# Performance work log

Hardware: AMD Instinct MI355X
Metric: run time of the kernel (lower is better)

Reference implementation:

```python
import jax, jax.numpy as jnp
import numpy as np

B, S, P, D = 32, 128, 64, 256   # batch, seq_len, pad_size, input_size
H, NF = 128, 3                   # hidden_size, n_filters
BI = 2                           # bidirectional -> b=2
OUT = 2                          # output_size
INITRANGE = 0.05


def setup_inputs() -> dict:
    key = jax.random.key(0)
    ks = jax.random.split(key, 17)
    u = lambda k, shape: jax.random.uniform(k, shape, jnp.float32, -INITRANGE, INITRANGE)
    return {
        "inputs": jax.random.normal(ks[0], (B, S, P, D), jnp.float32),
        "inputs_demoip": jax.random.normal(ks[1], (B, 3), jnp.float32),
        # Conv1d(1,1,kernel=D) collapses to a single dot product + scalar bias
        "conv_w": u(ks[2], (D,)),
        "conv_b": u(ks[3], ()),
        # Conv1d(1,NF,kernel=H*BI) collapses to NF dot products + bias
        "conv2_w": u(ks[4], (NF, H * BI)),
        "conv2_b": u(ks[5], (NF,)),
        # GRU params, forward and backward directions (PyTorch gate order r,z,n)
        "W_ih_f": u(ks[6], (3 * H, D)),
        "W_hh_f": u(ks[7], (3 * H, H)),
        "b_ih_f": u(ks[8], (3 * H,)),
        "b_hh_f": u(ks[9], (3 * H,)),
        "W_ih_b": u(ks[10], (3 * H, D)),
        "W_hh_b": u(ks[11], (3 * H, H)),
        "b_ih_b": u(ks[12], (3 * H,)),
        "b_hh_b": u(ks[13], (3 * H,)),
        "lin_w": u(ks[14], (OUT, H * BI * NF + 3)),
        "lin_b": u(ks[15], (OUT,)),
        "batch_size": B,
    }


def _gru_dir(x_seq, W_ih, W_hh, b_ih, b_hh, reverse):
    """Single-direction GRU, PyTorch semantics. x_seq: [B,S,D] -> [B,S,H]."""
    xg = jnp.einsum('bsd,gd->bsg', x_seq, W_ih) + b_ih  # [B,S,3H] precomputed input gates

    def step(h, xg_t):
        hg = h @ W_hh.T + b_hh
        xr, xz, xn = jnp.split(xg_t, 3, axis=-1)
        hr, hz, hn = jnp.split(hg, 3, axis=-1)
        r = jax.nn.sigmoid(xr + hr)
        z = jax.nn.sigmoid(xz + hz)
        n = jnp.tanh(xn + r * hn)
        h_new = (1.0 - z) * n + z * h
        return h_new, h_new

    h0 = jnp.zeros((x_seq.shape[0], W_hh.shape[1]), x_seq.dtype)
    _, hs = jax.lax.scan(step, h0, jnp.swapaxes(xg, 0, 1), reverse=reverse)
    return jnp.swapaxes(hs, 0, 1)


def reference(inputs, inputs_demoip, conv_w, conv_b, conv2_w, conv2_b,
              W_ih_f, W_hh_f, b_ih_f, b_hh_f,
              W_ih_b, W_hh_b, b_ih_b, b_hh_b,
              lin_w, lin_b, batch_size):
    # --- convolutional attention pooling over pad dim (fused, no per-step loop) ---
    scores = jnp.einsum('bspd,d->bsp', inputs, conv_w) + conv_b      # [B,S,P]
    conv_wts = jax.nn.softmax(scores, axis=-1)                        # [B,S,P]
    convolutions = jnp.einsum('bsp,bspd->bsd', conv_wts, inputs)      # [B,S,D]
    # --- bidirectional GRU (eval mode: dropout is identity) ---
    hf = _gru_dir(convolutions, W_ih_f, W_hh_f, b_ih_f, b_hh_f, False)
    hb = _gru_dir(convolutions, W_ih_b, W_hh_b, b_ih_b, b_hh_b, True)
    states_rnn = jnp.concatenate([hf, hb], axis=-1)                   # [B,S,2H]
    # --- second attention (conv2 over states, softmax over time per filter) ---
    alpha_scores = jnp.einsum('bsh,fh->bfs', states_rnn, conv2_w) + conv2_b[None, :, None]
    alpha = jax.nn.softmax(alpha_scores, axis=-1)                     # [B,NF,S]
    context = jnp.einsum('bfs,bsh->bfh', alpha, states_rnn).reshape(states_rnn.shape[0], -1)
    context_v2 = jnp.concatenate([context, inputs_demoip], axis=1)    # [B, 2H*NF+3]
    out = jax.nn.softmax(context_v2 @ lin_w.T + lin_b, axis=-1)       # [B,OUT]
    return out, alpha, states_rnn, context, conv_wts
```

## Files before the change

### kernel.cpp

```cpp
#include <hip/hip_runtime.h>
#include <hip/hip_bf16.h>

#define BB 32
#define SS 128
#define PP 64
#define DD 256
#define HH 128
#define NF 3

__global__ __launch_bounds__(256) void k_pool(
    const float* __restrict__ inp,
    const float* __restrict__ conv_w,
    const float* __restrict__ conv_bp,
    float* __restrict__ conv_out,
    float* __restrict__ conv_wts_out)
{
    __shared__ float scores[PP];
    __shared__ float wts[PP];
    __shared__ float4 part4[256];

    const int bs   = blockIdx.x;
    const int t    = threadIdx.x;
    const int lane = t & 63;
    const int wv   = t >> 6;

    const float4* src = reinterpret_cast<const float4*>(inp + (size_t)bs * (PP * DD));
    const float4  cw  = reinterpret_cast<const float4*>(conv_w)[lane];
    const float   cb  = conv_bp[0];

    float4 v[16];
#pragma unroll
    for (int i = 0; i < 16; ++i) v[i] = src[i * 256 + t];

    float part[16];
#pragma unroll
    for (int i = 0; i < 16; ++i)
        part[i] = v[i].x * cw.x + v[i].y * cw.y + v[i].z * cw.z + v[i].w * cw.w;

#pragma unroll
    for (int i = 0; i < 16; ++i) {
#pragma unroll
        for (int m = 32; m >= 1; m >>= 1) part[i] += __shfl_xor(part[i], m);
        if (lane == i) scores[i * 4 + wv] = part[i] + cb;
    }
    __syncthreads();

    if (wv == 0) {
        float s = scores[lane];
        float mx = s;
#pragma unroll
        for (int m = 32; m >= 1; m >>= 1) mx = fmaxf(mx, __shfl_xor(mx, m));
        float e = __expf(s - mx);
        float sm = e;
#pragma unroll
        for (int m = 32; m >= 1; m >>= 1) sm += __shfl_xor(sm, m);
        float w = e / sm;
        wts[lane] = w;
        conv_wts_out[(size_t)bs * PP + lane] = w;
    }
    __syncthreads();

    float4 acc = {0.f, 0.f, 0.f, 0.f};
#pragma unroll
    for (int i = 0; i < 16; ++i) {
        const float w = wts[4 * i + wv];
        acc.x = fmaf(w, v[i].x, acc.x);
        acc.y = fmaf(w, v[i].y, acc.y);
        acc.z = fmaf(w, v[i].z, acc.z);
        acc.w = fmaf(w, v[i].w, acc.w);
    }
    part4[t] = acc;
    __syncthreads();

    if (wv == 0) {
        float4 a = part4[lane];
        const float4 b1 = part4[64 + lane];
        const float4 b2 = part4[128 + lane];
        const float4 b3 = part4[192 + lane];
        a.x += b1.x + b2.x + b3.x;
        a.y += b1.y + b2.y + b3.y;
        a.z += b1.z + b2.z + b3.z;
        a.w += b1.w + b2.w + b3.w;
        reinterpret_cast<float4*>(conv_out + (size_t)bs * DD)[lane] = a;
    }
}

#define GBM 128
#define GBN 128
#define GBK 32
#define GAS 132

__global__ __launch_bounds__(256) void k_xg(
    const float* __restrict__ A,
    const float* __restrict__ Wf,
    const float* __restrict__ Wb,
    const float* __restrict__ bf,
    const float* __restrict__ bb,
    float* __restrict__ xg)
{
    __shared__ float as_[GBK * GAS];
    __shared__ float bs_[GBK * GAS];

    const int t  = threadIdx.x;
    const int i0 = blockIdx.x * GBM;
    const int j0 = blockIdx.y * GBN;
    const int tx = t & 15, ty = t >> 4;

    const float* Wsrc = (j0 < 384) ? (Wf + (size_t)j0 * DD) : (Wb + (size_t)(j0 - 384) * DD);
    const float* bsrc = (j0 < 384) ? (bf + j0) : (bb + (j0 - 384));

    float acc[8][8];
#pragma unroll
    for (int ii = 0; ii < 8; ++ii)
#pragma unroll
        for (int jj = 0; jj < 8; ++jj) acc[ii][jj] = 0.f;

    float4 pa[4], pb[4];
#pragma unroll
    for (int p = 0; p < 4; ++p) {
        const int idx = p * 256 + t, r = idx >> 3, k4 = idx & 7;
        pa[p] = *reinterpret_cast<const float4*>(&A[(size_t)(i0 + r) * DD + k4 * 4]);
        pb[p] = *reinterpret_cast<const float4*>(&Wsrc[(size_t)r * DD + k4 * 4]);
    }

    for (int kt = 0; kt < DD; kt += GBK) {
#pragma unroll
        for (int p = 0; p < 4; ++p) {
            const int idx = p * 256 + t, r = idx >> 3, k4 = idx & 7;
            as_[(k4 * 4 + 0) * GAS + r] = pa[p].x;
            as_[(k4 * 4 + 1) * GAS + r] = pa[p].y;
            as_[(k4 * 4 + 2) * GAS + r] = pa[p].z;
            as_[(k4 * 4 + 3) * GAS + r] = pa[p].w;
            bs_[(k4 * 4 + 0) * GAS + r] = pb[p].x;
            bs_[(k4 * 4 + 1) * GAS + r] = pb[p].y;
            bs_[(k4 * 4 + 2) * GAS + r] = pb[p].z;
            bs_[(k4 * 4 + 3) * GAS + r] = pb[p].w;
        }
        __syncthreads();
        if (kt + GBK < DD) {
#pragma unroll
            for (int p = 0; p < 4; ++p) {
                const int idx = p * 256 + t, r = idx >> 3, k4 = idx & 7;
                pa[p] = *reinterpret_cast<const float4*>(&A[(size_t)(i0 + r) * DD + kt + GBK + k4 * 4]);
                pb[p] = *reinterpret_cast<const float4*>(&Wsrc[(size_t)r * DD + kt + GBK + k4 * 4]);
            }
        }
#pragma unroll 8
        for (int k = 0; k < GBK; ++k) {
            float a[8], bq[8];
            *reinterpret_cast<float4*>(&a[0])  = *reinterpret_cast<const float4*>(&as_[k * GAS + ty * 8]);
            *reinterpret_cast<float4*>(&a[4])  = *reinterpret_cast<const float4*>(&as_[k * GAS + ty * 8 + 4]);
            *reinterpret_cast<float4*>(&bq[0]) = *reinterpret_cast<const float4*>(&bs_[k * GAS + tx * 4]);
            *reinterpret_cast<float4*>(&bq[4]) = *reinterpret_cast<const float4*>(&bs_[k * GAS + 64 + tx * 4]);
#pragma unroll
            for (int ii = 0; ii < 8; ++ii)
#pragma unroll
                for (int jj = 0; jj < 8; ++jj) acc[ii][jj] += a[ii] * bq[jj];
        }
        __syncthreads();
    }

    float bias[8];
#pragma unroll
    for (int jj = 0; jj < 4; ++jj) {
        bias[jj]     = bsrc[tx * 4 + jj];
        bias[4 + jj] = bsrc[64 + tx * 4 + jj];
    }
#pragma unroll
    for (int ii = 0; ii < 8; ++ii) {
        float* dst = &xg[(size_t)(i0 + ty * 8 + ii) * 768 + j0];
        float4 o0, o1;
        o0.x = acc[ii][0] + bias[0]; o0.y = acc[ii][1] + bias[1];
        o0.z = acc[ii][2] + bias[2]; o0.w = acc[ii][3] + bias[3];
        o1.x = acc[ii][4] + bias[4]; o1.y = acc[ii][5] + bias[5];
        o1.z = acc[ii][6] + bias[6]; o1.w = acc[ii][7] + bias[7];
        reinterpret_cast<float4*>(dst + tx * 4)[0]      = o0;
        reinterpret_cast<float4*>(dst + 64 + tx * 4)[0] = o1;
    }
}

__device__ __forceinline__ float sigm(float x) { return 1.f / (1.f + __expf(-x)); }
__device__ __forceinline__ float tanh_f(float x) { return 2.f / (1.f + __expf(-2.f * x)) - 1.f; }

template<int CTRL>
__device__ __forceinline__ float dpp_mov(float x) {
    return __int_as_float(__builtin_amdgcn_update_dpp(
        0, __float_as_int(x), CTRL, 0xF, 0xF, true));
}
#define DPP_XOR1 0xB1
#define DPP_XOR2 0x4E
#define DPP_HMIR 0x141

#define HSEG16 20
#define CH 16
#define XROW 384

__global__ __launch_bounds__(512) void k_gru(
    const float* __restrict__ xg,
    const float* __restrict__ Whf,
    const float* __restrict__ Whb,
    const float* __restrict__ bhf,
    const float* __restrict__ bhb,
    float* __restrict__ states)
{
    const int blk = blockIdx.x;
    const int b   = blk >> 1;
    const int dir = blk & 1;
    const int tid = threadIdx.x;
    const int g   = tid >> 3;
    const int p   = tid & 7;

    __shared__ float hb[2][8 * HSEG16];
    __shared__ float xs[2][CH * XROW];
    __shared__ float sring[2][CH][HH];

    const float* Wh = dir ? Whb : Whf;
    const float* bh = dir ? bhb : bhf;

    const int j = g + 64 * ((p >> 2) & 1);
    const bool gate = (p & 3) == 0;
    float bhr = 0.f, bhz = 0.f, bhn = 0.f;
    if (gate) { bhr = bh[j]; bhz = bh[HH + j]; bhn = bh[2 * HH + j]; }

    float4 wra[4], wrb[4], wza[4], wzb[4], wna[4], wnb[4];
    {
        const float4* p_ra = reinterpret_cast<const float4*>(Wh + (size_t)g * HH + p * 16);
        const float4* p_rb = reinterpret_cast<const float4*>(Wh + (size_t)(g + 64) * HH + p * 16);
        const float4* p_za = reinterpret_cast<const float4*>(Wh + (size_t)(HH + g) * HH + p * 16);
        const float4* p_zb = reinterpret_cast<const float4*>(Wh + (size_t)(HH + g + 64) * HH + p * 16);
        const float4* p_na = reinterpret_cast<const float4*>(Wh + (size_t)(2 * HH + g) * HH + p * 16);
        const float4* p_nb = reinterpret_cast<const float4*>(Wh + (size_t)(2 * HH + g + 64) * HH + p * 16);
#pragma unroll
        for (int k = 0; k < 4; ++k) {
            wra[k] = p_ra[k]; wrb[k] = p_rb[k];
            wza[k] = p_za[k]; wzb[k] = p_zb[k];
            wna[k] = p_na[k]; wnb[k] = p_nb[k];
        }
    }

    const float* xg_bd = xg + (size_t)b * SS * 768 + dir * 384;
    const int hidx = (j >> 4) * HSEG16 + (j & 15);

    float4 pf[3];
#pragma unroll
    for (int j3 = 0; j3 < 3; ++j3) {
        const int flat4 = j3 * 512 + tid;
        const int sic = flat4 / 96, w4 = flat4 % 96;
        const int s = dir ? (SS - 1 - sic) : sic;
        pf[j3] = *reinterpret_cast<const float4*>(xg_bd + (size_t)s * 768 + w4 * 4);
    }
#pragma unroll
    for (int j3 = 0; j3 < 3; ++j3) {
        const int flat4 = j3 * 512 + tid;
        const int sic = flat4 / 96, w4 = flat4 % 96;
        *reinterpret_cast<float4*>(&xs[0][sic * XROW + w4 * 4]) = pf[j3];
    }
    if (tid < 8 * HSEG16) hb[0][tid] = 0.f;
    __syncthreads();
#pragma unroll
    for (int j3 = 0; j3 < 3; ++j3) {
        const int flat4 = j3 * 512 + tid;
        const int sic = flat4 / 96, w4 = flat4 % 96;
        const int stp = CH + sic;
        const int s = dir ? (SS - 1 - stp) : stp;
        pf[j3] = *reinterpret_cast<const float4*>(xg_bd + (size_t)s * 768 + w4 * 4);
    }

    for (int step = 0; step < SS; ++step) {
        const int cur = step & 1;
        const int sic = step & (CH - 1);
        const int buf = (step >> 4) & 1;

        const float* hrow = hb[cur];
        float4 hq[4];
#pragma unroll
        for (int k = 0; k < 4; ++k)
            hq[k] = *reinterpret_cast<const float4*>(&hrow[p * HSEG16 + k * 4]);

        float hp = 0.f, xrv = 0.f, xzv = 0.f, xnv = 0.f;
        if (gate) {
            hp  = hrow[hidx];
            xrv = xs[buf][sic * XROW + j];
            xzv = xs[buf][sic * XROW + HH + j];
            xnv = xs[buf][sic * XROW + 2 * HH + j];
        }

        float a_ra = 0.f, a_rb = 0.f, a_za = 0.f, a_zb = 0.f, a_na = 0.f, a_nb = 0.f;
#pragma unroll
        for (int k = 0; k < 4; ++k) {
            const float4 h4 = hq[k];
            a_ra = fmaf(wra[k].x, h4.x, a_ra); a_ra = fmaf(wra[k].y, h4.y, a_ra);
            a_ra = fmaf(wra[k].z, h4.z, a_ra); a_ra = fmaf(wra[k].w, h4.w, a_ra);
            a_rb = fmaf(wrb[k].x, h4.x, a_rb); a_rb = fmaf(wrb[k].y, h4.y, a_rb);
            a_rb = fmaf(wrb[k].z, h4.z, a_rb); a_rb = fmaf(wrb[k].w, h4.w, a_rb);
            a_za = fmaf(wza[k].x, h4.x, a_za); a_za = fmaf(wza[k].y, h4.y, a_za);
            a_za = fmaf(wza[k].z, h4.z, a_za); a_za = fmaf(wza[k].w, h4.w, a_za);
            a_zb = fmaf(wzb[k].x, h4.x, a_zb); a_zb = fmaf(wzb[k].y, h4.y, a_zb);
            a_zb = fmaf(wzb[k].z, h4.z, a_zb); a_zb = fmaf(wzb[k].w, h4.w, a_zb);
            a_na = fmaf(wna[k].x, h4.x, a_na); a_na = fmaf(wna[k].y, h4.y, a_na);
            a_na = fmaf(wna[k].z, h4.z, a_na); a_na = fmaf(wna[k].w, h4.w, a_na);
            a_nb = fmaf(wnb[k].x, h4.x, a_nb); a_nb = fmaf(wnb[k].y, h4.y, a_nb);
            a_nb = fmaf(wnb[k].z, h4.z, a_nb); a_nb = fmaf(wnb[k].w, h4.w, a_nb);
        }

        const bool own_b = (tid & 4) != 0;
        const float s_r = own_b ? a_ra : a_rb;
        const float s_z = own_b ? a_za : a_zb;
        const float s_n = own_b ? a_na : a_nb;
        float f_r = (own_b ? a_rb : a_ra) + dpp_mov<DPP_HMIR>(s_r);
        float f_z = (own_b ? a_zb : a_za) + dpp_mov<DPP_HMIR>(s_z);
        float f_n = (own_b ? a_nb : a_na) + dpp_mov<DPP_HMIR>(s_n);
        f_r += dpp_mov<DPP_XOR1>(f_r);
        f_z += dpp_mov<DPP_XOR1>(f_z);
        f_n += dpp_mov<DPP_XOR1>(f_n);
        f_r += dpp_mov<DPP_XOR2>(f_r);
        f_z += dpp_mov<DPP_XOR2>(f_z);
        f_n += dpp_mov<DPP_XOR2>(f_n);

        if (gate) {
            const float r = sigm(xrv + f_r + bhr);
            const float z = sigm(xzv + f_z + bhz);
            const float n = tanh_f(xnv + r * (f_n + bhn));
            const float hnew = (1.f - z) * n + z * hp;
            hb[cur ^ 1][hidx] = hnew;
            sring[buf][sic][j] = hnew;
        }

        if (sic == CH - 1 && step != SS - 1) {
#pragma unroll
            for (int j3 = 0; j3 < 3; ++j3) {
                const int flat4 = j3 * 512 + tid;
                const int sc = flat4 / 96, w4 = flat4 % 96;
                *reinterpret_cast<float4*>(&xs[buf ^ 1][sc * XROW + w4 * 4]) = pf[j3];
            }
        }
        __syncthreads();

        if (sic == CH - 1) {
            const int cb   = (step >> 4) * CH;
            const int sic2 = tid >> 5;
            const int off  = (tid & 31) * 4;
            const int st   = cb + sic2;
            const int sO   = dir ? (SS - 1 - st) : st;
            const float4 v4 = *reinterpret_cast<const float4*>(&sring[buf][sic2][off]);
            *reinterpret_cast<float4*>(&states[((size_t)b * SS + sO) * 256 + dir * HH + off]) = v4;
            if (step + CH + 1 < SS) {
                const int nchunk = (step >> 4) + 2;
#pragma unroll
                for (int j3 = 0; j3 < 3; ++j3) {
                    const int flat4 = j3 * 512 + tid;
                    const int sc = flat4 / 96, w4 = flat4 % 96;
                    const int st2 = nchunk * CH + sc;
                    const int s2 = dir ? (SS - 1 - st2) : st2;
                    pf[j3] = *reinterpret_cast<const float4*>(xg_bd + (size_t)s2 * 768 + w4 * 4);
                }
            }
        }
    }
}

__global__ __launch_bounds__(256) void k_attn2(
    const float* __restrict__ states,
    const float* __restrict__ c2w,
    const float* __restrict__ c2b,
    const float* __restrict__ demoip,
    const float* __restrict__ lin_w,
    const float* __restrict__ lin_b,
    float* __restrict__ out,
    float* __restrict__ alpha_out,
    float* __restrict__ ctx_out)
{
    const int b    = blockIdx.x;
    const int t    = threadIdx.x;
    const int lane = t & 63;
    const int wv   = t >> 6;

    __shared__ float sc[NF * SS];
    __shared__ float al[NF * SS];
    __shared__ float pbuf[4][NF * 256];
    __shared__ float ctx[768];

    const float* st = states + (size_t)b * SS * 256;

    for (int o = t; o < NF * SS; o += 256) {
        const int f = o >> 7, s = o & 127;
        const float4* r4 = reinterpret_cast<const float4*>(st + (size_t)s * 256);
        const float4* w4 = reinterpret_cast<const float4*>(c2w + f * 256);
        float a0 = 0.f, a1 = 0.f, a2 = 0.f, a3 = 0.f;
#pragma unroll
        for (int k = 0; k < 64; k += 4) {
            const float4 x0 = r4[k],     y0 = w4[k];
            const float4 x1 = r4[k + 1], y1 = w4[k + 1];
            const float4 x2 = r4[k + 2], y2 = w4[k + 2];
            const float4 x3 = r4[k + 3], y3 = w4[k + 3];
            a0 = fmaf(x0.x, y0.x, a0); a0 = fmaf(x0.y, y0.y, a0);
            a0 = fmaf(x0.z, y0.z, a0); a0 = fmaf(x0.w, y0.w, a0);
            a1 = fmaf(x1.x, y1.x, a1); a1 = fmaf(x1.y, y1.y, a1);
            a1 = fmaf(x1.z, y1.z, a1); a1 = fmaf(x1.w, y1.w, a1);
            a2 = fmaf(x2.x, y2.x, a2); a2 = fmaf(x2.y, y2.y, a2);
            a2 = fmaf(x2.z, y2.z, a2); a2 = fmaf(x2.w, y2.w, a2);
            a3 = fmaf(x3.x, y3.x, a3); a3 = fmaf(x3.y, y3.y, a3);
            a3 = fmaf(x3.z, y3.z, a3); a3 = fmaf(x3.w, y3.w, a3);
        }
        sc[o] = ((a0 + a1) + (a2 + a3)) + c2b[f];
    }
    __syncthreads();

    if (wv < NF) {
        const float v0 = sc[wv * SS + lane], v1 = sc[wv * SS + 64 + lane];
        float mx = fmaxf(v0, v1);
#pragma unroll
        for (int m = 32; m >= 1; m >>= 1) mx = fmaxf(mx, __shfl_xor(mx, m));
        const float e0 = __expf(v0 - mx), e1 = __expf(v1 - mx);
        float sm = e0 + e1;
#pragma unroll
        for (int m = 32; m >= 1; m >>= 1) sm += __shfl_xor(sm, m);
        const float r = 1.f / sm;
        al[wv * SS + lane]      = e0 * r;
        al[wv * SS + 64 + lane] = e1 * r;
        alpha_out[((size_t)b * NF + wv) * SS + lane]      = e0 * r;
        alpha_out[((size_t)b * NF + wv) * SS + 64 + lane] = e1 * r;
    }
    __syncthreads();

    {
        const int grp = t >> 6, h4 = t & 63;
        float4 c0 = {0,0,0,0}, c1 = {0,0,0,0}, c2 = {0,0,0,0};
#pragma unroll 4
        for (int i = 0; i < 32; ++i) {
            const int s = grp * 32 + i;
            const float4 sv = *reinterpret_cast<const float4*>(st + (size_t)s * 256 + h4 * 4);
            const float a0 = al[s], a1 = al[SS + s], a2 = al[2 * SS + s];
            c0.x = fmaf(a0, sv.x, c0.x); c0.y = fmaf(a0, sv.y, c0.y);
            c0.z = fmaf(a0, sv.z, c0.z); c0.w = fmaf(a0, sv.w, c0.w);
            c1.x = fmaf(a1, sv.x, c1.x); c1.y = fmaf(a1, sv.y, c1.y);
            c1.z = fmaf(a1, sv.z, c1.z); c1.w = fmaf(a1, sv.w, c1.w);
            c2.x = fmaf(a2, sv.x, c2.x); c2.y = fmaf(a2, sv.y, c2.y);
            c2.z = fmaf(a2, sv.z, c2.z); c2.w = fmaf(a2, sv.w, c2.w);
        }
        *reinterpret_cast<float4*>(&pbuf[grp][0 * 256 + h4 * 4]) = c0;
        *reinterpret_cast<float4*>(&pbuf[grp][1 * 256 + h4 * 4]) = c1;
        *reinterpret_cast<float4*>(&pbuf[grp][2 * 256 + h4 * 4]) = c2;
    }
    __syncthreads();

    for (int o = t; o < 768; o += 256) {
        const float v = pbuf[0][o] + pbuf[1][o] + pbuf[2][o] + pbuf[3][o];
        ctx[o] = v;
        ctx_out[(size_t)b * 768 + o] = v;
    }
    __syncthreads();

    if (wv == 0) {
        const float* lw0 = lin_w;
        const float* lw1 = lin_w + 771;
        float a0 = 0.f, a1 = 0.f;
#pragma unroll 4
        for (int i = lane; i < 768; i += 64) {
            const float c = ctx[i];
            a0 = fmaf(c, lw0[i], a0);
            a1 = fmaf(c, lw1[i], a1);
        }
#pragma unroll
        for (int m = 32; m >= 1; m >>= 1) {
            a0 += __shfl_xor(a0, m);
            a1 += __shfl_xor(a1, m);
        }
        if (lane == 0) {
            a0 += lin_b[0]; a1 += lin_b[1];
            for (int k = 0; k < 3; ++k) {
                const float d = demoip[b * 3 + k];
                a0 = fmaf(d, lw0[768 + k], a0);
                a1 = fmaf(d, lw1[768 + k], a1);
            }
            const float m  = fmaxf(a0, a1);
            const float e0 = __expf(a0 - m), e1 = __expf(a1 - m);
            const float s  = e0 + e1;
            out[b * 2 + 0] = e0 / s;
            out[b * 2 + 1] = e1 / s;
        }
    }
}

extern "C" void kernel_launch(void* const* d_in, const int* in_sizes, int n_in,
                              void* d_out, int out_size, void* d_ws, size_t ws_size,
                              hipStream_t stream) {
    const float* inp     = (const float*)d_in[0];
    const float* demoip  = (const float*)d_in[1];
    const float* conv_w  = (const float*)d_in[2];
    const float* conv_b  = (const float*)d_in[3];
    const float* c2w     = (const float*)d_in[4];
    const float* c2b     = (const float*)d_in[5];
    const float* Wih_f   = (const float*)d_in[6];
    const float* Whh_f   = (const float*)d_in[7];
    const float* bih_f   = (const float*)d_in[8];
    const float* bhh_f   = (const float*)d_in[9];
    const float* Wih_b   = (const float*)d_in[10];
    const float* Whh_b   = (const float*)d_in[11];
    const float* bih_b   = (const float*)d_in[12];
    const float* bhh_b   = (const float*)d_in[13];
    const float* lin_w   = (const float*)d_in[14];
    const float* lin_b   = (const float*)d_in[15];

    float* out      = (float*)d_out;
    float* alpha    = out + 64;
    float* states   = out + 12352;
    float* context  = out + 1060928;
    float* conv_wts = out + 1085504;

    float* conv_out = (float*)d_ws;
    float* xg       = conv_out + (size_t)4096 * 256;

    k_pool<<<dim3(BB * SS), dim3(256), 0, stream>>>(inp, conv_w, conv_b, conv_out, conv_wts);
    k_xg<<<dim3(4096 / GBM, 768 / GBN), dim3(256), 0, stream>>>(conv_out, Wih_f, Wih_b, bih_f, bih_b, xg);
    k_gru<<<dim3(64), dim3(512), 0, stream>>>(xg, Whh_f, Whh_b, bhh_f, bhh_b, states);
    k_attn2<<<dim3(BB), dim3(256), 0, stream>>>(states, c2w, c2b, demoip, lin_w, lin_b, out, alpha, context);
}
```

Before: 199.6 us.

## Fuse conv2 attention scores into GRU epilogue and widen attn2 block

Each GRU block now computes its direction's partial conv2 score for every 16-step chunk straight from the shared-memory state ring, using DPP reductions. The partials go to workspace that reuses the conv_out buffer, which is dead once k_xg has run. k_attn2 then only sums the two direction partials plus the bias, instead of re-reading all states for the score dot products. k_attn2 also moves to 512 threads, so the context reduction runs over 8 groups of 16 timesteps. The cost is extra work inside the latency-bound GRU chunk boundary, which may stretch the serial recurrence.

```diff
diff --git a/kernel.cpp b/kernel.cpp
--- a/kernel.cpp
+++ b/kernel.cpp
@@ -7,6 +7,7 @@
 #define DD 256
 #define HH 128
 #define NF 3
+
 
 __global__ __launch_bounds__(256) void k_pool(
     const float* __restrict__ inp,
@@ -201,7 +202,9 @@
     const float* __restrict__ Whb,
     const float* __restrict__ bhf,
     const float* __restrict__ bhb,
-    float* __restrict__ states)
+    const float* __restrict__ c2w,
+    float* __restrict__ states,
+    float* __restrict__ sc_part)
 {
     const int blk = blockIdx.x;
     const int b   = blk >> 1;
@@ -337,13 +340,38 @@
         __syncthreads();
 
         if (sic == CH - 1) {
-            const int cb   = (step >> 4) * CH;
-            const int sic2 = tid >> 5;
-            const int off  = (tid & 31) * 4;
-            const int st   = cb + sic2;
-            const int sO   = dir ? (SS - 1 - st) : st;
-            const float4 v4 = *reinterpret_cast<const float4*>(&sring[buf][sic2][off]);
-            *reinterpret_cast<float4*>(&states[((size_t)b * SS + sO) * 256 + dir * HH + off]) = v4;
+            const int cb = (step >> 4) * CH;
+            {
+                const int sic2 = tid >> 5;
+                const int off  = (tid & 31) * 4;
+                const int st   = cb + sic2;
+                const int sO   = dir ? (SS - 1 - st) : st;
+                const float4 v4 = *reinterpret_cast<const float4*>(&sring[buf][sic2][off]);
+                *reinterpret_cast<float4*>(&states[((size_t)b * SS + sO) * 256 + dir * HH + off]) = v4;
+            }
+            if (tid < 384) {
+                const int pair = tid >> 3;
+                const int sl   = pair & 15;
+                const int f    = pair >> 4;
+                const int l8   = tid & 7;
+                const float4* h4p = reinterpret_cast<const float4*>(&sring[buf][sl][l8 * 16]);
+                const float4* w4p = reinterpret_cast<const float4*>(c2w + f * 256 + dir * HH + l8 * 16);
+                float a = 0.f;
+#pragma unroll
+                for (int k = 0; k < 4; ++k) {
+                    const float4 hv = h4p[k], wv4 = w4p[k];
+                    a = fmaf(hv.x, wv4.x, a); a = fmaf(hv.y, wv4.y, a);
+                    a = fmaf(hv.z, wv4.z, a); a = fmaf(hv.w, wv4.w, a);
+                }
+                a += dpp_mov<DPP_XOR1>(a);
+                a += dpp_mov<DPP_XOR2>(a);
+                a += dpp_mov<DPP_HMIR>(a);
+                if (l8 == 0) {
+                    const int st = cb + sl;
+                    const int sO = dir ? (SS - 1 - st) : st;
+                    sc_part[(((size_t)b * 2 + dir) * NF + f) * SS + sO] = a;
+                }
+            }
             if (step + CH + 1 < SS) {
                 const int nchunk = (step >> 4) + 2;
 #pragma unroll
@@ -359,9 +387,9 @@
     }
 }
 
-__global__ __launch_bounds__(256) void k_attn2(
+__global__ __launch_bounds__(512) void k_attn2(
     const float* __restrict__ states,
-    const float* __restrict__ c2w,
+    const float* __restrict__ sc_part,
     const float* __restrict__ c2b,
     const float* __restrict__ demoip,
     const float* __restrict__ lin_w,
@@ -377,32 +405,16 @@
 
     __shared__ float sc[NF * SS];
     __shared__ float al[NF * SS];
-    __shared__ float pbuf[4][NF * 256];
+    __shared__ float pbuf[8][NF * 256];
     __shared__ float ctx[768];
 
     const float* st = states + (size_t)b * SS * 256;
 
-    for (int o = t; o < NF * SS; o += 256) {
-        const int f = o >> 7, s = o & 127;
-        const float4* r4 = reinterpret_cast<const float4*>(st + (size_t)s * 256);
-        const float4* w4 = reinterpret_cast<const float4*>(c2w + f * 256);
-        float a0 = 0.f, a1 = 0.f, a2 = 0.f, a3 = 0.f;
-#pragma unroll
-        for (int k = 0; k < 64; k += 4) {
-            const float4 x0 = r4[k],     y0 = w4[k];
-            const float4 x1 = r4[k + 1], y1 = w4[k + 1];
-            const float4 x2 = r4[k + 2], y2 = w4[k + 2];
-            const float4 x3 = r4[k + 3], y3 = w4[k + 3];
-            a0 = fmaf(x0.x, y0.x, a0); a0 = fmaf(x0.y, y0.y, a0);
-            a0 = fmaf(x0.z, y0.z, a0); a0 = fmaf(x0.w, y0.w, a0);
-            a1 = fmaf(x1.x, y1.x, a1); a1 = fmaf(x1.y, y1.y, a1);
-            a1 = fmaf(x1.z, y1.z, a1); a1 = fmaf(x1.w, y1.w, a1);
-            a2 = fmaf(x2.x, y2.x, a2); a2 = fmaf(x2.y, y2.y, a2);
-            a2 = fmaf(x2.z, y2.z, a2); a2 = fmaf(x2.w, y2.w, a2);
-            a3 = fmaf(x3.x, y3.x, a3); a3 = fmaf(x3.y, y3.y, a3);
-            a3 = fmaf(x3.z, y3.z, a3); a3 = fmaf(x3.w, y3.w, a3);
-        }
-        sc[o] = ((a0 + a1) + (a2 + a3)) + c2b[f];
+    if (t < NF * SS) {
+        const int f = t >> 7, s = t & 127;
+        sc[t] = sc_part[(((size_t)b * 2 + 0) * NF + f) * SS + s]
+              + sc_part[(((size_t)b * 2 + 1) * NF + f) * SS + s]
+              + c2b[f];
     }
     __syncthreads();
 
@@ -427,8 +439,8 @@
         const int grp = t >> 6, h4 = t & 63;
         float4 c0 = {0,0,0,0}, c1 = {0,0,0,0}, c2 = {0,0,0,0};
 #pragma unroll 4
-        for (int i = 0; i < 32; ++i) {
-            const int s = grp * 32 + i;
+        for (int i = 0; i < 16; ++i) {
+            const int s = grp * 16 + i;
             const float4 sv = *reinterpret_cast<const float4*>(st + (size_t)s * 256 + h4 * 4);
             const float a0 = al[s], a1 = al[SS + s], a2 = al[2 * SS + s];
             c0.x = fmaf(a0, sv.x, c0.x); c0.y = fmaf(a0, sv.y, c0.y);
@@ -444,8 +456,10 @@
     }
     __syncthreads();
 
-    for (int o = t; o < 768; o += 256) {
-        const float v = pbuf[0][o] + pbuf[1][o] + pbuf[2][o] + pbuf[3][o];
+    for (int o = t; o < 768; o += 512) {
+        float v = 0.f;
+#pragma unroll
+        for (int k = 0; k < 8; ++k) v += pbuf[k][o];
         ctx[o] = v;
         ctx_out[(size_t)b * 768 + o] = v;
     }
@@ -510,9 +524,10 @@
 
     float* conv_out = (float*)d_ws;
     float* xg       = conv_out + (size_t)4096 * 256;
+    float* sc_part  = conv_out;
 
     k_pool<<<dim3(BB * SS), dim3(256), 0, stream>>>(inp, conv_w, conv_b, conv_out, conv_wts);
     k_xg<<<dim3(4096 / GBM, 768 / GBN), dim3(256), 0, stream>>>(conv_out, Wih_f, Wih_b, bih_f, bih_b, xg);
-    k_gru<<<dim3(64), dim3(512), 0, stream>>>(xg, Whh_f, Whh_b, bhh_f, bhh_b, states);
-    k_attn2<<<dim3(BB), dim3(256), 0, stream>>>(states, c2w, c2b, demoip, lin_w, lin_b, out, alpha, context);
+    k_gru<<<dim3(64), dim3(512), 0, stream>>>(xg, Whh_f, Whh_b, bhh_f, bhh_b, c2w, states, sc_part);
+    k_attn2<<<dim3(BB), dim3(512), 0, stream>>>(states, sc_part, c2b, demoip, lin_w, lin_b, out, alpha, context);
 }
```

Result: faster. 187.8 us (-5.9%).
